# Optimization experiments

Hardware: AMD Instinct MI355X
Metric: run time of the kernel (lower is better)

Reference implementation:

```python
import jax, jax.numpy as jnp
import numpy as np

C = 512
GROUPS = 32
EPS = 1e-6


def setup_inputs() -> dict:
    key = jax.random.key(0)
    ks = jax.random.split(key, 12)
    B, H, W = 4, 64, 64
    s = 1.0 / np.sqrt(C)
    return {
        "x": jax.random.normal(ks[0], (B, C, H, W), dtype=jnp.float32),
        "gn_w": jnp.ones((C,), jnp.float32),
        "gn_b": jnp.zeros((C,), jnp.float32),
        "wq": jax.random.normal(ks[1], (C, C), jnp.float32) * s,
        "bq": jnp.zeros((C,), jnp.float32),
        "wk": jax.random.normal(ks[2], (C, C), jnp.float32) * s,
        "bk": jnp.zeros((C,), jnp.float32),
        "wv": jax.random.normal(ks[3], (C, C), jnp.float32) * s,
        "bv": jnp.zeros((C,), jnp.float32),
        "wp": jax.random.normal(ks[4], (C, C), jnp.float32) * s,
        "bp": jnp.zeros((C,), jnp.float32),
    }


def _group_norm(x, w, b):
    B, Cc, H, W = x.shape
    xg = x.reshape(B, GROUPS, Cc // GROUPS, H, W)
    mu = xg.mean(axis=(2, 3, 4), keepdims=True)
    var = xg.var(axis=(2, 3, 4), keepdims=True)
    xg = (xg - mu) * jax.lax.rsqrt(var + EPS)
    xn = xg.reshape(B, Cc, H, W)
    return xn * w[None, :, None, None] + b[None, :, None, None]


def _conv1x1(x, w, b):
    # x: (B,C,H,W), w: (O,C) -> (B,O,H,W)
    return jnp.einsum('bchw,oc->bohw', x, w) + b[None, :, None, None]


def reference(x, gn_w, gn_b, wq, bq, wk, bk, wv, bv, wp, bp):
    B, Cc, H, W = x.shape
    N = H * W
    scale = Cc ** (-0.5)
    h_ = _group_norm(x, gn_w, gn_b)
    q = _conv1x1(h_, wq, bq).reshape(B, Cc, N)  # (B,C,N)
    k = _conv1x1(h_, wk, bk).reshape(B, Cc, N)
    v = _conv1x1(h_, wv, bv).reshape(B, Cc, N)
    # scores[b,i,j] = sum_c q[b,c,i] * k[b,c,j]
    attn = jnp.einsum('bci,bcj->bij', q, k) * scale  # (B,N,N)
    attn = jax.nn.softmax(attn, axis=2)
    # h_[b,c,i] = sum_j v[b,c,j] * attn[b,i,j]
    h2 = jnp.einsum('bcj,bij->bci', v, attn).reshape(B, Cc, H, W)
    return x + _conv1x1(h2, wp, bp)
```

## Files before the change

kernel.cpp:

```cpp
#include <hip/hip_runtime.h>

#define NPIX 4096
#define CCH  512
#define NGRP 32
#define BATCH 4
#define NT   64

using bf16 = __bf16;
typedef __bf16 bf16x8 __attribute__((ext_vector_type(8)));
typedef __bf16 bf16x4 __attribute__((ext_vector_type(4)));
typedef float  f32x4  __attribute__((ext_vector_type(4)));

__device__ __forceinline__ f32x4 mfma16(bf16x8 a, bf16x8 b, f32x4 c) {
    return __builtin_amdgcn_mfma_f32_16x16x32_bf16(a, b, c, 0, 0, 0);
}

__device__ __forceinline__ void gld_lds16(const void* g, void* l) {
    __builtin_amdgcn_global_load_lds(
        (const __attribute__((address_space(1))) unsigned int*)g,
        (__attribute__((address_space(3))) unsigned int*)l,
        16, 0, 0);
}

__device__ __forceinline__ void swz_src(int l, int& drow, int& dcol) {
    int m = (l & 7) ^ (l >> 3);
    drow = 2 * (l >> 3) + (m >> 2);
    dcol = (m & 3) * 8;
}
__device__ __forceinline__ int swz_roff(int c, int g) {
    return ((c >> 1) << 6) + ((((((c & 1) << 2) | g)) ^ ((c >> 1) & 7)) << 3);
}

__global__ __launch_bounds__(256) void cvt_all(const float* __restrict__ wq,
                                               const float* __restrict__ wk,
                                               const float* __restrict__ wv,
                                               const float* __restrict__ wp,
                                               bf16* __restrict__ d, float cscale) {
    int i = blockIdx.x * 256 + threadIdx.x;
    int seg = i >> 16;
    const float* s = (seg == 0) ? wq : (seg == 1) ? wk : (seg == 2) ? wv : wp;
    float scale = (seg == 0) ? cscale : 1.f;
    float4 v = ((const float4*)s)[i & 65535];
    bf16x4 o;
    o[0] = (bf16)(v.x*scale); o[1] = (bf16)(v.y*scale);
    o[2] = (bf16)(v.z*scale); o[3] = (bf16)(v.w*scale);
    ((bf16x4*)d)[i] = o;
}

__global__ __launch_bounds__(256) void gn_stats(const float* __restrict__ x, float2* __restrict__ stats) {
    int bg = blockIdx.x;
    const float4* p = (const float4*)(x + (size_t)bg * 65536);
    float s = 0.f, ss = 0.f;
    for (int i = threadIdx.x; i < 16384; i += 256) {
        float4 v = p[i];
        s  += v.x + v.y + v.z + v.w;
        ss += v.x*v.x + v.y*v.y + v.z*v.z + v.w*v.w;
    }
    __shared__ float r1[256], r2[256];
    int t = threadIdx.x;
    r1[t] = s; r2[t] = ss;
    __syncthreads();
    for (int st = 128; st > 0; st >>= 1) {
        if (t < st) { r1[t] += r1[t+st]; r2[t] += r2[t+st]; }
        __syncthreads();
    }
    if (t == 0) {
        float mu  = r1[0] * (1.f/65536.f);
        float var = r2[0] * (1.f/65536.f) - mu*mu;
        stats[bg] = make_float2(mu, rsqrtf(var + 1e-6f));
    }
}

__global__ __launch_bounds__(256) void gn_norm_t(const float* __restrict__ x,
                                                 const float2* __restrict__ stats,
                                                 const float* __restrict__ gw,
                                                 const float* __restrict__ gb,
                                                 bf16* __restrict__ hnt) {
    __shared__ float tile[64][65];
    int n0 = blockIdx.x * 64, c0 = blockIdx.y * 64, b = blockIdx.z;
    int t = threadIdx.x;
    {
        int cr = t >> 4;
        int nc = (t & 15) * 4;
        #pragma unroll
        for (int rep = 0; rep < 4; ++rep) {
            int c = c0 + rep*16 + cr;
            float2 st = stats[b*NGRP + (c >> 4)];
            float w = gw[c], bb = gb[c];
            float4 v = *(const float4*)(x + ((size_t)b*CCH + c)*NPIX + n0 + nc);
            float* dst = &tile[rep*16 + cr][nc];
            dst[0] = (v.x - st.x)*st.y*w + bb;
            dst[1] = (v.y - st.x)*st.y*w + bb;
            dst[2] = (v.z - st.x)*st.y*w + bb;
            dst[3] = (v.w - st.x)*st.y*w + bb;
        }
    }
    __syncthreads();
    {
        int nr = t >> 2;
        int cp = (t & 3) * 16;
        bf16x8 o0, o1;
        #pragma unroll
        for (int j = 0; j < 8; ++j) {
            o0[j] = (bf16)tile[cp + j    ][nr];
            o1[j] = (bf16)tile[cp + 8 + j][nr];
        }
        bf16* dst = hnt + ((size_t)b*NPIX + n0 + nr)*CCH + c0 + cp;
        *(bf16x8*)dst       = o0;
        *((bf16x8*)dst + 1) = o1;
    }
}

__global__ __launch_bounds__(256, 2)
void gemm_qkv(const bf16* __restrict__ Wcat, const bf16* __restrict__ X,
              const float* __restrict__ bq, const float* __restrict__ bk,
              const float* __restrict__ bv, bf16* __restrict__ qt,
              bf16* __restrict__ kt, bf16* __restrict__ vch, float cscale) {
    __shared__ bf16 tX[2][4096];
    __shared__ bf16 tW[2][4096];
    int n0 = blockIdx.x * 128, o0g = blockIdx.y * 128, b = blockIdx.z;
    int seg = o0g >> 9, osel = o0g & 511;
    const float* bias = (seg == 0) ? bq : (seg == 1) ? bk : bv;
    bf16* Yb = (seg == 0) ? qt : (seg == 1) ? kt : vch;
    float osc = (seg == 0) ? cscale : 1.f;
    bool vmode = (seg == 2);

    int t = threadIdx.x, lane = t & 63, w = t >> 6;
    int wm = (w >> 1) * 64, wn = (w & 1) * 64;
    int col = lane & 15, g = lane >> 4;
    int roff = swz_roff(col, g);
    int drow, dcol;
    swz_src(lane, drow, dcol);
    f32x4 acc[4][4] = {};
    const bf16* gX = X + ((size_t)b*NPIX + n0) * CCH;
    const bf16* gW = Wcat + (size_t)o0g * CCH;

    auto stage = [&](int buf, int k0) {
        #pragma unroll
        for (int i = 0; i < 2; ++i) {
            int rb = (w*2 + i) * 16;
            gld_lds16(gX + (size_t)(rb + drow)*CCH + k0 + dcol, &tX[buf][rb*32]);
            gld_lds16(gW + (size_t)(rb + drow)*CCH + k0 + dcol, &tW[buf][rb*32]);
        }
    };

    stage(0, 0);
    __syncthreads();

    for (int it = 0; it < 16; ++it) {
        int buf = it & 1;
        if (it < 15) stage(buf ^ 1, (it + 1) * 32);
        bf16x8 fA[4], fB[4];
        #pragma unroll
        for (int i = 0; i < 4; ++i) {
            if (!vmode) {
                fA[i] = *(bf16x8*)&tX[buf][(wm + i*16)*32 + roff];
                fB[i] = *(bf16x8*)&tW[buf][(wn + i*16)*32 + roff];
            } else {
                fA[i] = *(bf16x8*)&tW[buf][(wm + i*16)*32 + roff];
                fB[i] = *(bf16x8*)&tX[buf][(wn + i*16)*32 + roff];
            }
        }
        #pragma unroll
        for (int i = 0; i < 4; ++i)
            #pragma unroll
            for (int j = 0; j < 4; ++j)
                acc[i][j] = mfma16(fA[i], fB[j], acc[i][j]);
        __syncthreads();
    }

    int row4 = g * 4;
    #pragma unroll
    for (int i = 0; i < 4; ++i) {
        #pragma unroll
        for (int j = 0; j < 4; ++j) {
            #pragma unroll
            for (int r = 0; r < 4; ++r) {
                float vv = acc[i][j][r];
                int m = wm + i*16 + row4 + r;
                int n = wn + j*16 + col;
                if (!vmode) {
                    int sp = n0 + m, o = osel + n;
                    Yb[((size_t)b*NPIX + sp)*CCH + o] = (bf16)(vv + osc*bias[o]);
                } else {
                    int o = osel + m, sp = n0 + n;
                    Yb[((size_t)b*CCH + o)*NPIX + sp] = (bf16)(vv + bias[o]);
                }
            }
        }
    }
}

__global__ __launch_bounds__(256, 2)
void gemm_proj(const bf16* __restrict__ W, const bf16* __restrict__ X,
               const float* __restrict__ bias, float* __restrict__ Yf,
               const float* __restrict__ resid) {
    __shared__ bf16 tX[2][4096];
    __shared__ bf16 tW[2][4096];
    int n0 = blockIdx.x * 128, o0 = blockIdx.y * 128, b = blockIdx.z;
    int t = threadIdx.x, lane = t & 63, w = t >> 6;
    int wm = (w >> 1) * 64, wn = (w & 1) * 64;
    int col = lane & 15, g = lane >> 4;
    int roff = swz_roff(col, g);
    int drow, dcol;
    swz_src(lane, drow, dcol);
    f32x4 acc[4][4] = {};
    const bf16* gX = X + ((size_t)b*NPIX + n0) * CCH;
    const bf16* gW = W + (size_t)o0 * CCH;

    auto stage = [&](int buf, int k0) {
        #pragma unroll
        for (int i = 0; i < 2; ++i) {
            int rb = (w*2 + i) * 16;
            gld_lds16(gX + (size_t)(rb + drow)*CCH + k0 + dcol, &tX[buf][rb*32]);
            gld_lds16(gW + (size_t)(rb + drow)*CCH + k0 + dcol, &tW[buf][rb*32]);
        }
    };

    stage(0, 0);
    __syncthreads();

    for (int it = 0; it < 16; ++it) {
        int buf = it & 1;
        if (it < 15) stage(buf ^ 1, (it + 1) * 32);
        bf16x8 fA[4], fB[4];
        #pragma unroll
        for (int i = 0; i < 4; ++i) {
            fA[i] = *(bf16x8*)&tW[buf][(wm + i*16)*32 + roff];
            fB[i] = *(bf16x8*)&tX[buf][(wn + i*16)*32 + roff];
        }
        #pragma unroll
        for (int i = 0; i < 4; ++i)
            #pragma unroll
            for (int j = 0; j < 4; ++j)
                acc[i][j] = mfma16(fA[i], fB[j], acc[i][j]);
        __syncthreads();
    }

    int row4 = g * 4;
    #pragma unroll
    for (int i = 0; i < 4; ++i) {
        #pragma unroll
        for (int j = 0; j < 4; ++j) {
            #pragma unroll
            for (int r = 0; r < 4; ++r) {
                int o = o0 + wm + i*16 + row4 + r;
                int sp = n0 + wn + j*16 + col;
                size_t idx = ((size_t)b*CCH + o)*NPIX + sp;
                Yf[idx] = acc[i][j][r] + bias[o] + resid[idx];
            }
        }
    }
}

__global__ __launch_bounds__(512, 2)
void attn_flash(const bf16* __restrict__ qt, const bf16* __restrict__ kt,
                const bf16* __restrict__ v, bf16* __restrict__ pacc0,
                bf16* __restrict__ pacc1, float* __restrict__ lsum) {
    __shared__ bf16 Kt[2][16384];
    __shared__ bf16 Vt[2][16384];
    __shared__ bf16 Pl[8][16][40];
    __shared__ float Ls[128];

    const int L  = blockIdx.x + 32 * blockIdx.y + 128 * blockIdx.z;
    const int gx = L & 7, ix = L >> 3;
    const int b  = gx & 3, jz = gx >> 2;

    const int t = threadIdx.x, lane = t & 63, w = t >> 6;
    const int q0 = ix * 128 + w * 16;
    const int col = lane & 15, g = lane >> 4, kq = g * 8;
    const int jbase = jz * 2048;

    const bf16* kbase = kt + (size_t)b*NPIX*CCH;
    const bf16* vbase = v  + (size_t)b*CCH*NPIX;
    int drow, dcol; swz_src(lane, drow, dcol);
    const int kx0 = (col & 7) << 4;
    const int vro = 2*swz_roff(col, g);

    bf16x8 qf[16];
    {
        const bf16* qrow = qt + ((size_t)b*NPIX + q0 + col)*CCH + kq;
        #pragma unroll
        for (int kk = 0; kk < 16; ++kk) qf[kk] = *(const bf16x8*)(qrow + kk*32);
    }

    auto stage = [&](int buf, int j0) {
        #pragma unroll
        for (int i = 0; i < 4; ++i) {
            int row = w*4 + i;
            gld_lds16((const char*)(kbase + (size_t)(j0 + row)*CCH) + ((lane*16) ^ ((row & 7) << 4)),
                      (char*)&Kt[buf][0] + row*1024);
        }
        #pragma unroll
        for (int i = 0; i < 4; ++i) {
            int blk = w*4 + i;
            gld_lds16(vbase + (size_t)(blk*16 + drow)*NPIX + j0 + dcol,
                      (char*)&Vt[buf][0] + blk*1024);
        }
    };

    stage(0, jbase);
    __syncthreads();

    f32x4 acc[8][4] = {};
    float lacc[4] = {0.f, 0.f, 0.f, 0.f};

    for (int it = 0; it < NT; ++it) {
        const int buf = it & 1;
        if (it < NT-1) stage(buf ^ 1, jbase + (it + 1) * 32);

        f32x4 s0a = {}, s0b = {}, s1a = {}, s1b = {};
        const char* kb0 = (const char*)&Kt[buf][0] + col*1024;
        const char* kb1 = kb0 + 16*1024;
        #pragma unroll
        for (int kk = 0; kk < 16; kk += 2) {
            int e0 = (kk*64     + g*16) ^ kx0;
            int e1 = ((kk+1)*64 + g*16) ^ kx0;
            s0a = mfma16(qf[kk],   *(const bf16x8*)(kb0 + e0), s0a);
            s1a = mfma16(qf[kk],   *(const bf16x8*)(kb1 + e0), s1a);
            s0b = mfma16(qf[kk+1], *(const bf16x8*)(kb0 + e1), s0b);
            s1b = mfma16(qf[kk+1], *(const bf16x8*)(kb1 + e1), s1b);
        }
        f32x4 s0 = s0a + s0b;
        f32x4 s1 = s1a + s1b;

        #pragma unroll
        for (int r = 0; r < 4; ++r) {
            float p0 = __expf(s0[r]);
            float p1 = __expf(s1[r]);
            lacc[r] += p0 + p1;
            Pl[w][g*4 + r][col]      = (bf16)p0;
            Pl[w][g*4 + r][col + 16] = (bf16)p1;
        }

        asm volatile("s_waitcnt lgkmcnt(0)" ::: "memory");
        asm volatile("s_barrier" ::: "memory");
        __builtin_amdgcn_sched_barrier(0);

        const char* vb = (const char*)&Vt[buf][0] + (w << 12);
        bf16x8 bv0 = *(const bf16x8*)(vb          + vro);
        bf16x8 bv1 = *(const bf16x8*)(vb + 1024   + vro);
        bf16x8 bv2 = *(const bf16x8*)(vb + 2048   + vro);
        bf16x8 bv3 = *(const bf16x8*)(vb + 3072   + vro);
        #pragma unroll
        for (int qtl = 0; qtl < 8; ++qtl) {
            bf16x8 pa = *(bf16x8*)&Pl[qtl][col][kq];
            acc[qtl][0] = mfma16(pa, bv0, acc[qtl][0]);
            acc[qtl][1] = mfma16(pa, bv1, acc[qtl][1]);
            acc[qtl][2] = mfma16(pa, bv2, acc[qtl][2]);
            acc[qtl][3] = mfma16(pa, bv3, acc[qtl][3]);
        }
        __syncthreads();
    }

    #pragma unroll
    for (int r = 0; r < 4; ++r) {
        float s = lacc[r];
        #pragma unroll
        for (int off = 1; off < 16; off <<= 1) s += __shfl_xor(s, off);
        if (col == 0) {
            Ls[w*16 + g*4 + r] = 1.f / s;
            lsum[((size_t)jz*BATCH + b)*NPIX + q0 + g*4 + r] = s;
        }
    }
    __syncthreads();

    bf16* pout = jz ? pacc1 : pacc0;
    const int q0b = ix * 128;
    #pragma unroll
    for (int qtl = 0; qtl < 8; ++qtl) {
        f32x4 rlq = *(const f32x4*)&Ls[qtl*16 + g*4];
        #pragma unroll
        for (int i = 0; i < 4; ++i) {
            int ch = w*64 + i*16 + col;
            bf16x4 ov;
            #pragma unroll
            for (int r = 0; r < 4; ++r) ov[r] = (bf16)(acc[qtl][i][r] * rlq[r]);
            *(bf16x4*)(pout + ((size_t)b*CCH + ch)*NPIX + q0b + qtl*16 + g*4) = ov;
        }
    }
}

__global__ __launch_bounds__(256)
void merge_t(const bf16* __restrict__ p0, const bf16* __restrict__ p1,
             const float* __restrict__ lsum, bf16* __restrict__ h2t) {
    __shared__ float tile[64][65];
    __shared__ float w0s[64], w1s[64];
    int n0 = blockIdx.x * 64, c0 = blockIdx.y * 64, b = blockIdx.z;
    int t = threadIdx.x;
    if (t < 64) {
        float l0 = lsum[(size_t)b*NPIX + n0 + t];
        float l1 = lsum[(size_t)(BATCH + b)*NPIX + n0 + t];
        float inv = 1.f / (l0 + l1);
        w0s[t] = l0 * inv; w1s[t] = l1 * inv;
    }
    __syncthreads();
    {
        int cl = t >> 2, nc = (t & 3) * 16;
        size_t base = ((size_t)b*CCH + c0 + cl)*NPIX + n0 + nc;
        #pragma unroll
        for (int h = 0; h < 2; ++h) {
            bf16x8 a0 = *(const bf16x8*)(p0 + base + h*8);
            bf16x8 a1 = *(const bf16x8*)(p1 + base + h*8);
            #pragma unroll
            for (int j = 0; j < 8; ++j)
                tile[cl][nc + h*8 + j] = (float)a0[j]*w0s[nc + h*8 + j]
                                       + (float)a1[j]*w1s[nc + h*8 + j];
        }
    }
    __syncthreads();
    {
        int nr = t >> 2, cp = (t & 3) * 16;
        bf16x8 o0, o1;
        #pragma unroll
        for (int j = 0; j < 8; ++j) {
            o0[j] = (bf16)tile[cp + j    ][nr];
            o1[j] = (bf16)tile[cp + 8 + j][nr];
        }
        bf16* dst = h2t + ((size_t)b*NPIX + n0 + nr)*CCH + c0 + cp;
        *(bf16x8*)dst       = o0;
        *((bf16x8*)dst + 1) = o1;
    }
}

extern "C" void kernel_launch(void* const* d_in, const int* in_sizes, int n_in,
                              void* d_out, int out_size, void* d_ws, size_t ws_size,
                              hipStream_t stream) {
    (void)in_sizes; (void)n_in; (void)out_size; (void)ws_size;
    const float* x   = (const float*)d_in[0];
    const float* gnw = (const float*)d_in[1];
    const float* gnb = (const float*)d_in[2];
    const float* wq  = (const float*)d_in[3];
    const float* bq  = (const float*)d_in[4];
    const float* wk  = (const float*)d_in[5];
    const float* bk  = (const float*)d_in[6];
    const float* wv  = (const float*)d_in[7];
    const float* bv  = (const float*)d_in[8];
    const float* wp  = (const float*)d_in[9];
    const float* bp  = (const float*)d_in[10];
    const float cscale = 0.04419417382415922f;

    char* ws = (char*)d_ws;
    bf16* wcat = (bf16*)ws;
    bf16* wpb  = wcat + 3*262144;
    float2* stats = (float2*)(ws + 4*524288);
    const size_t TEN = (size_t)BATCH*NPIX*CCH;
    bf16* hnt = (bf16*)(ws + 4*524288 + 4096);
    bf16* qt  = hnt + TEN;
    bf16* kt  = qt  + TEN;
    bf16* vch = kt  + TEN;
    bf16* pacc1 = vch + TEN;
    float* lsum = (float*)(pacc1 + TEN);
    bf16* pacc0 = hnt;
    bf16* h2t   = qt;

    cvt_all<<<1024, 256, 0, stream>>>(wq, wk, wv, wp, wcat, cscale);

    gn_stats<<<BATCH*NGRP, 256, 0, stream>>>(x, stats);
    gn_norm_t<<<dim3(NPIX/64, CCH/64, BATCH), 256, 0, stream>>>(x, stats, gnw, gnb, hnt);

    gemm_qkv<<<dim3(NPIX/128, 12, BATCH), 256, 0, stream>>>(
        wcat, hnt, bq, bk, bv, qt, kt, vch, cscale);

    attn_flash<<<dim3(32, BATCH, 2), 512, 0, stream>>>(qt, kt, vch, pacc0, pacc1, lsum);

    merge_t<<<dim3(NPIX/64, CCH/64, BATCH), 256, 0, stream>>>(pacc0, pacc1, lsum, h2t);

    gemm_proj<<<dim3(NPIX/128, CCH/128, BATCH), 256, 0, stream>>>(
        wpb, h2t, bp, (float*)d_out, x);
}
```

Before: 336.5 us.

## Software-pipeline attention loop: overlap QK^T/exp of next tile with PV of previous

Restructures the flash-attention main loop so the P·V MFMAs for tile it-1 run in the same iteration as the QK^T and exp for tile it. The P scratch tile is double-buffered in LDS, with a prologue and an epilogue added. This removes the mid-iteration barrier, leaving one barrier per iteration, and gives the scheduler independent MFMA streams to interleave. The cost is extra LDS for the second P buffer and slightly more code, which could affect occupancy at 2 blocks per CU.

```diff
diff --git a/kernel.cpp b/kernel.cpp
--- a/kernel.cpp
+++ b/kernel.cpp
@@ -259,7 +259,7 @@
                 bf16* __restrict__ pacc1, float* __restrict__ lsum) {
     __shared__ bf16 Kt[2][16384];
     __shared__ bf16 Vt[2][16384];
-    __shared__ bf16 Pl[8][16][40];
+    __shared__ bf16 Pl[2][8][16][40];
     __shared__ float Ls[128];
 
     const int L  = blockIdx.x + 32 * blockIdx.y + 128 * blockIdx.z;
@@ -299,16 +299,10 @@
         }
     };
 
-    stage(0, jbase);
-    __syncthreads();
-
     f32x4 acc[8][4] = {};
     float lacc[4] = {0.f, 0.f, 0.f, 0.f};
 
-    for (int it = 0; it < NT; ++it) {
-        const int buf = it & 1;
-        if (it < NT-1) stage(buf ^ 1, jbase + (it + 1) * 32);
-
+    auto qkt_exp = [&](int buf) {
         f32x4 s0a = {}, s0b = {}, s1a = {}, s1b = {};
         const char* kb0 = (const char*)&Kt[buf][0] + col*1024;
         const char* kb1 = kb0 + 16*1024;
@@ -323,34 +317,63 @@
         }
         f32x4 s0 = s0a + s0b;
         f32x4 s1 = s1a + s1b;
-
         #pragma unroll
         for (int r = 0; r < 4; ++r) {
             float p0 = __expf(s0[r]);
             float p1 = __expf(s1[r]);
             lacc[r] += p0 + p1;
-            Pl[w][g*4 + r][col]      = (bf16)p0;
-            Pl[w][g*4 + r][col + 16] = (bf16)p1;
-        }
-
-        asm volatile("s_waitcnt lgkmcnt(0)" ::: "memory");
-        asm volatile("s_barrier" ::: "memory");
-        __builtin_amdgcn_sched_barrier(0);
-
-        const char* vb = (const char*)&Vt[buf][0] + (w << 12);
+            Pl[buf][w][g*4 + r][col]      = (bf16)p0;
+            Pl[buf][w][g*4 + r][col + 16] = (bf16)p1;
+        }
+    };
+
+    stage(0, jbase);
+    __syncthreads();
+
+    stage(1, jbase + 32);
+    qkt_exp(0);
+    __syncthreads();
+
+    for (int it = 1; it < NT; ++it) {
+        const int buf = it & 1, pb = buf ^ 1;
+
+        const char* vb = (const char*)&Vt[pb][0] + (w << 12);
         bf16x8 bv0 = *(const bf16x8*)(vb          + vro);
         bf16x8 bv1 = *(const bf16x8*)(vb + 1024   + vro);
         bf16x8 bv2 = *(const bf16x8*)(vb + 2048   + vro);
         bf16x8 bv3 = *(const bf16x8*)(vb + 3072   + vro);
+        asm volatile("s_waitcnt lgkmcnt(0)" ::: "memory");
+        __builtin_amdgcn_sched_barrier(0);
+
+        if (it < NT-1) stage(pb, jbase + (it + 1) * 32);
+
         #pragma unroll
         for (int qtl = 0; qtl < 8; ++qtl) {
-            bf16x8 pa = *(bf16x8*)&Pl[qtl][col][kq];
+            bf16x8 pa = *(bf16x8*)&Pl[pb][qtl][col][kq];
             acc[qtl][0] = mfma16(pa, bv0, acc[qtl][0]);
             acc[qtl][1] = mfma16(pa, bv1, acc[qtl][1]);
             acc[qtl][2] = mfma16(pa, bv2, acc[qtl][2]);
             acc[qtl][3] = mfma16(pa, bv3, acc[qtl][3]);
         }
+
+        qkt_exp(buf);
         __syncthreads();
+    }
+
+    {
+        const char* vb = (const char*)&Vt[1][0] + (w << 12);
+        bf16x8 bv0 = *(const bf16x8*)(vb          + vro);
+        bf16x8 bv1 = *(const bf16x8*)(vb + 1024   + vro);
+        bf16x8 bv2 = *(const bf16x8*)(vb + 2048   + vro);
+        bf16x8 bv3 = *(const bf16x8*)(vb + 3072   + vro);
+        #pragma unroll
+        for (int qtl = 0; qtl < 8; ++qtl) {
+            bf16x8 pa = *(bf16x8*)&Pl[1][qtl][col][kq];
+            acc[qtl][0] = mfma16(pa, bv0, acc[qtl][0]);
+            acc[qtl][1] = mfma16(pa, bv1, acc[qtl][1]);
+            acc[qtl][2] = mfma16(pa, bv2, acc[qtl][2]);
+            acc[qtl][3] = mfma16(pa, bv3, acc[qtl][3]);
+        }
     }
 
     #pragma unroll
```

Result: faster. 293.5 us (-12.8%).
